# Performance work log

Hardware: AMD Instinct MI355X
Metric: run time of the kernel (lower is better)

The kernel has to match this reference:

```python
import jax, jax.numpy as jnp
import numpy as np

N, E, P, L, F, H, T = 6000, 72000, 2, 2, 64, 4, 64
NF_MLP = 256
DH = F // H
M = (L + 1) ** 2  # 9 spherical components for max_degree=2
DEG = np.array([l for l in range(L + 1) for _ in range(2 * l + 1)])  # degree of each m-component
EPS = 1e-6


def _deg_dense(x, W):
    # x: (n,P,M,Fin); W: (P,L+1,Fin,Fout). Separate feature mixing per (parity, degree),
    return jnp.einsum('npmf,pmfg->npmg', x, W[:, DEG])


def _eqv_layernorm(x):
    # Equivariant LayerNorm (no scale/bias): center the scalar (l=0) channel over features,
    # then divide each (parity, degree) block by the RMS (over features) of its per-degree norm.
    s = x[:, :, 0:1, :]
    x = x.at[:, :, 0:1, :].set(s - s.mean(axis=-1, keepdims=True))
    n2 = jnp.stack([(x[:, :, l * l:(l + 1) * (l + 1), :] ** 2).sum(axis=2) / (2 * l + 1)
                    for l in range(L + 1)], axis=2)  # (n,P,L+1,F)
    rms = jnp.sqrt(n2.mean(axis=-1, keepdims=True) + EPS)  # (n,P,L+1,1)
    return x / rms[:, :, DEG, :]


def _modulate(x, scale, shift):
    # modulate_E3adaLN: x * (1 + gamma) with gamma broadcast per degree; shift only on l=0 (scalar).
    y = x * (1.0 + scale[:, :, DEG, :])
    return y.at[:, :, 0:1, :].add(shift)


def _gate(factor, t):
    # broadcast_equivariant_multiplication: per-(parity,degree,feature) factor broadcast over m.
    return factor[:, :, DEG, :] * t


def _eqv_gelu(x):
    s = x[:, 0:1, 0:1, :]
    mask = jnp.abs(s) > 1e-4
    safe = jnp.where(mask, s, 1.0)
    g = jnp.where(mask, jax.nn.gelu(safe) / safe, 0.5)
    return x * g


def _forward(features_nodes, features_edges, features_time, cutoff_value,
             ln_t_scale, ln_t_bias, W_c, b_c, Wq, Wk, Wv, Wo, We_qk, We_v, W1, W2,
             src_idx, dst_idx):
    n = features_nodes.shape[0]
    # ---- AdaLN conditioning from time features ----
    mu = features_time.mean(-1, keepdims=True)
    var = ((features_time - mu) ** 2).mean(-1, keepdims=True)
    c = (features_time - mu) / jnp.sqrt(var + EPS) * ln_t_scale + ln_t_bias
    c = jax.nn.silu(c) @ W_c + b_c  # (n, 4*F*(L+1)*P + 2F)
    a = F * (L + 1) * P  # 384
    g1, b1, a1, g2, b2, a2 = jnp.split(c, [a, a + F, 2 * a + F, 3 * a + F, 3 * a + 2 * F], axis=-1)
    g1 = g1.reshape(n, P, L + 1, F); b1 = b1.reshape(n, 1, 1, F); a1 = a1.reshape(n, P, L + 1, F)
    g2 = g2.reshape(n, P, L + 1, F); b2 = b2.reshape(n, 1, 1, F); a2 = a2.reshape(n, P, L + 1, F)
    x_pre = _modulate(_eqv_layernorm(features_nodes), g1, b1)
    # ---- sparse graph equivariant self-attention ----
    q = _deg_dense(x_pre, Wq).reshape(n, P, M, H, DH)
    k = _deg_dense(x_pre, Wk).reshape(n, P, M, H, DH)
    v = _deg_dense(x_pre, Wv).reshape(n, P, M, H, DH)
    e_qk = jnp.einsum('eomf,fg->eomg', features_edges, We_qk).reshape(-1, 1, M, H, DH)
    e_v = jnp.einsum('eomf,fg->eomg', features_edges, We_v).reshape(-1, 1, M, H, DH)
    qe = q[dst_idx]
    ke = k[src_idx] * e_qk  # relative positional encoding on keys
    ve = v[src_idx] * e_v   # relative positional encoding on values
    logits = jnp.einsum('epmhd,epmhd->eh', qe, ke) / np.sqrt(P * M * DH)  # rotation-invariant
    lmax = jax.ops.segment_max(logits, dst_idx, num_segments=n)
    w = jnp.exp(logits - lmax[dst_idx]) * cutoff_value[:, None]  # cutoff-masked softmax weight
    denom = jax.ops.segment_sum(w, dst_idx, num_segments=n)
    attn = w / (denom[dst_idx] + 1e-9)  # (E,H)
    out = jax.ops.segment_sum(attn[:, None, None, :, None] * ve, dst_idx, num_segments=n)
    out = _deg_dense(out.reshape(n, P, M, F), Wo)
    # fallback to pre-attention features where segment_mean(cutoff) ~ 0 (isolated nodes)
    cnt = jax.ops.segment_sum(jnp.ones_like(cutoff_value), dst_idx, num_segments=n)
    mean_cut = jax.ops.segment_sum(cutoff_value, dst_idx, num_segments=n) / jnp.maximum(cnt, 1.0)
    post = jnp.where(mean_cut.reshape(-1, 1, 1, 1) < 1e-5, x_pre, out)
    x = features_nodes + _gate(a1, post)
    # ---- equivariant MLP ----
    x_pre2 = _modulate(_eqv_layernorm(x), g2, b2)
    h = _eqv_gelu(_deg_dense(x_pre2, W1))
    x = x + _gate(a2, _deg_dense(h, W2))
    return x  # node features; edge features pass through unchanged


def setup_inputs():
    key = jax.random.key(0)
    ks = jax.random.split(key, 16)
    CDIM = 4 * F * (L + 1) * P + 2 * F  # 1664
    return {
        'features_nodes': jax.random.normal(ks[0], (N, P, M, F), jnp.float32),
        'features_edges': jax.random.normal(ks[1], (E, 1, M, F), jnp.float32),
        'features_time': jax.random.normal(ks[2], (N, T), jnp.float32),
        'cutoff_value': jax.random.uniform(ks[3], (E,), jnp.float32),
        'ln_t_scale': jnp.ones((T,), jnp.float32),
        'ln_t_bias': jnp.zeros((T,), jnp.float32),
        'W_c': jax.random.normal(ks[4], (T, CDIM), jnp.float32) * 0.02,
        'b_c': jnp.zeros((CDIM,), jnp.float32),
        'Wq': jax.random.normal(ks[5], (P, L + 1, F, F), jnp.float32) / np.sqrt(F),
        'Wk': jax.random.normal(ks[6], (P, L + 1, F, F), jnp.float32) / np.sqrt(F),
        'Wv': jax.random.normal(ks[7], (P, L + 1, F, F), jnp.float32) / np.sqrt(F),
        'Wo': jax.random.normal(ks[8], (P, L + 1, F, F), jnp.float32) / np.sqrt(F),
        'We_qk': jax.random.normal(ks[9], (F, F), jnp.float32) / np.sqrt(F),
        'We_v': jax.random.normal(ks[10], (F, F), jnp.float32) / np.sqrt(F),
        'W1': jax.random.normal(ks[11], (P, L + 1, F, NF_MLP), jnp.float32) / np.sqrt(F),
        'W2': jax.random.normal(ks[12], (P, L + 1, NF_MLP, F), jnp.float32) / np.sqrt(NF_MLP),
        'src_idx': jax.random.randint(ks[13], (E,), 0, N),
        'dst_idx': jax.random.randint(ks[14], (E,), 0, N),
    }


def reference(features_nodes, features_edges, features_time, cutoff_value,
              ln_t_scale, ln_t_bias, W_c, b_c, Wq, Wk, Wv, Wo, We_qk, We_v, W1, W2,
              src_idx, dst_idx):
    return _forward(features_nodes, features_edges, features_time, cutoff_value,
                    ln_t_scale, ln_t_bias, W_c, b_c, Wq, Wk, Wv, Wo, We_qk, We_v, W1, W2,
                    src_idx, dst_idx)
```

## Files before the change

kernel.cpp:

```cpp
#include <hip/hip_runtime.h>
#include <hip/hip_fp16.h>
#include <math.h>


#define NN 6000
#define EE 72000

__device__ __forceinline__ float wsum(float v) {
#pragma unroll
  for (int o = 32; o >= 1; o >>= 1) v += __shfl_xor(v, o, 64);
  return v;
}
__device__ __forceinline__ int deg_of(int m) { return (m == 0) ? 0 : ((m < 4) ? 1 : 2); }
__device__ __forceinline__ unsigned fenc(float x) {
  unsigned u = __float_as_uint(x);
  return (u & 0x80000000u) ? ~u : (u | 0x80000000u);
}
__device__ __forceinline__ float fdec(unsigned k) {
  unsigned u = (k & 0x80000000u) ? (k & 0x7fffffffu) : ~k;
  return __uint_as_float(u);
}

__global__ __launch_bounds__(256) void k_ln_t(const float* __restrict__ ft,
                                              const float* __restrict__ lns,
                                              const float* __restrict__ lnb,
                                              float* __restrict__ sbuf) {
  int w = (blockIdx.x * 256 + threadIdx.x) >> 6;
  int lane = threadIdx.x & 63;
  float t = ft[(size_t)w * 64 + lane];
  float mu = wsum(t) * (1.f / 64.f);
  float d = t - mu;
  float var = wsum(d * d) * (1.f / 64.f);
  float cin = d * rsqrtf(var + 1e-6f) * lns[lane] + lnb[lane];
  sbuf[(size_t)w * 64 + lane] = cin / (1.f + expf(-cin));
}

__global__ __launch_bounds__(256) void k_cond_mm(const float* __restrict__ sbuf,
                                                 const float* __restrict__ Wc,
                                                 const float* __restrict__ bc,
                                                 float* __restrict__ c) {
  int n0 = blockIdx.x * 8;
  for (int jj = threadIdx.x; jj < 1664; jj += 256) {
    float acc[8] = {0, 0, 0, 0, 0, 0, 0, 0};
#pragma unroll 8
    for (int k2 = 0; k2 < 64; k2++) {
      float wv = Wc[(size_t)k2 * 1664 + jj];
#pragma unroll
      for (int nd = 0; nd < 8; nd++) acc[nd] += sbuf[(size_t)(n0 + nd) * 64 + k2] * wv;
    }
    float b = bc[jj];
#pragma unroll
    for (int nd = 0; nd < 8; nd++) c[(size_t)(n0 + nd) * 1664 + jj] = acc[nd] + b;
  }
}

__global__ __launch_bounds__(256) void k_lnmod(const float* __restrict__ xin,
                                               const float* __restrict__ c,
                                               float* __restrict__ xout,
                                               int goff, int boff) {
  int w = (blockIdx.x * 256 + threadIdx.x) >> 6;
  int lane = threadIdx.x & 63;
  int n = w >> 1, p = w & 1;
  const float* xb = xin + (size_t)w * 576 + lane;
  float x0 = xb[0], x1 = xb[64], x2 = xb[128], x3 = xb[192], x4 = xb[256];
  float x5 = xb[320], x6 = xb[384], x7 = xb[448], x8 = xb[512];
  float mu = wsum(x0) * (1.f / 64.f);
  x0 -= mu;
  float n20 = x0 * x0;
  float n21 = (x1 * x1 + x2 * x2 + x3 * x3) * (1.f / 3.f);
  float n22 = (x4 * x4 + x5 * x5 + x6 * x6 + x7 * x7 + x8 * x8) * (1.f / 5.f);
  n20 = wsum(n20) * (1.f / 64.f);
  n21 = wsum(n21) * (1.f / 64.f);
  n22 = wsum(n22) * (1.f / 64.f);
  float i0 = rsqrtf(n20 + 1e-6f), i1 = rsqrtf(n21 + 1e-6f), i2 = rsqrtf(n22 + 1e-6f);
  const float* cb = c + (size_t)n * 1664;
  float g0 = 1.f + cb[goff + p * 192 + lane];
  float g1 = 1.f + cb[goff + p * 192 + 64 + lane];
  float g2 = 1.f + cb[goff + p * 192 + 128 + lane];
  float bsh = cb[boff + lane];
  float* ob = xout + (size_t)w * 576 + lane;
  ob[0] = x0 * i0 * g0 + bsh;
  ob[64] = x1 * i1 * g1;
  ob[128] = x2 * i1 * g1;
  ob[192] = x3 * i1 * g1;
  ob[256] = x4 * i2 * g2;
  ob[320] = x5 * i2 * g2;
  ob[384] = x6 * i2 * g2;
  ob[448] = x7 * i2 * g2;
  ob[512] = x8 * i2 * g2;
}

__global__ __launch_bounds__(256) void k_count(const int* __restrict__ dst_idx,
                                               const float* __restrict__ cutoff,
                                               float* __restrict__ cnt,
                                               float* __restrict__ cutsum) {
  int e = blockIdx.x * 256 + threadIdx.x;
  if (e >= EE) return;
  int d = dst_idx[e];
  unsafeAtomicAdd(cnt + d, 1.f);
  unsafeAtomicAdd(cutsum + d, cutoff[e]);
}

__global__ __launch_bounds__(1024) void k_scan(const float* __restrict__ cnt,
                                               int* __restrict__ rowptr,
                                               int* __restrict__ fillc) {
  __shared__ int part[1024];
  int t = threadIdx.x;
  int base = t * 6;
  int lc[6];
  int s = 0;
#pragma unroll
  for (int i = 0; i < 6; i++) {
    int idx = base + i;
    int vv = (idx < NN) ? (int)(cnt[idx] + 0.5f) : 0;
    lc[i] = s;
    s += vv;
  }
  part[t] = s;
  __syncthreads();
  for (int o = 1; o < 1024; o <<= 1) {
    int vv = (t >= o) ? part[t - o] : 0;
    __syncthreads();
    part[t] += vv;
    __syncthreads();
  }
  int ex = (t == 0) ? 0 : part[t - 1];
#pragma unroll
  for (int i = 0; i < 6; i++) {
    int idx = base + i;
    if (idx < NN) {
      int p = ex + lc[i];
      rowptr[idx] = p;
      fillc[idx] = p;
    }
  }
  if (t == 1023) rowptr[NN] = part[1023];
}

__global__ __launch_bounds__(256) void k_fill(const int* __restrict__ dst_idx,
                                              const int* __restrict__ src_idx,
                                              const float* __restrict__ cutoff,
                                              int* __restrict__ fillc,
                                              int* __restrict__ eids,
                                              int* __restrict__ dsts,
                                              int* __restrict__ srcs,
                                              float* __restrict__ cuts) {
  int e = blockIdx.x * 256 + threadIdx.x;
  if (e >= EE) return;
  int d = dst_idx[e];
  int pos = atomicAdd(fillc + d, 1);
  eids[pos] = e;
  dsts[pos] = d;
  srcs[pos] = src_idx[e];
  cuts[pos] = cutoff[e];
}

__global__ __launch_bounds__(192) void k_qkv2(const float* __restrict__ xpre,
                                              const float* __restrict__ Wq,
                                              const float* __restrict__ Wk,
                                              const float* __restrict__ Wv,
                                              __half* __restrict__ qh,
                                              __half* __restrict__ kh,
                                              __half* __restrict__ vh) {
  __shared__ __align__(16) float xt[16 * 64];
  int pm = blockIdx.y;
  int p = pm / 9, dm = deg_of(pm % 9);
  int n0 = blockIdx.x * 16;
  int mat = threadIdx.x >> 6;
  int g = threadIdx.x & 63;
  for (int i = threadIdx.x; i < 1024; i += 192) {
    int r = i >> 6, f = i & 63;
    xt[i] = xpre[((size_t)(n0 + r) * 18 + pm) * 64 + f];
  }
  const float* Wsel = (mat == 0) ? Wq : ((mat == 1) ? Wk : Wv);
  const float* Wb = Wsel + (size_t)(p * 3 + dm) * 4096;
  __half* ob = (mat == 0) ? qh : ((mat == 1) ? kh : vh);
  float wreg[64];
#pragma unroll
  for (int f = 0; f < 64; f++) wreg[f] = Wb[f * 64 + g];
  __syncthreads();
  for (int r = 0; r < 16; r++) {
    float acc = 0.f;
#pragma unroll
    for (int f4 = 0; f4 < 16; f4++) {
      float4 a = *(const float4*)(xt + r * 64 + f4 * 4);
      acc += a.x * wreg[4 * f4] + a.y * wreg[4 * f4 + 1] + a.z * wreg[4 * f4 + 2] +
             a.w * wreg[4 * f4 + 3];
    }
    ob[((size_t)(n0 + r) * 18 + pm) * 64 + g] = __float2half(acc);
  }
}

__global__ __launch_bounds__(256) void k_edge(const float* __restrict__ fe,
                                              const float* __restrict__ Weqk,
                                              const float* __restrict__ Wev,
                                              const __half* __restrict__ qh,
                                              const __half* __restrict__ kh,
                                              const int* __restrict__ eids,
                                              const int* __restrict__ dsts,
                                              const int* __restrict__ srcs,
                                              __half* __restrict__ evh,
                                              float* __restrict__ logw,
                                              unsigned* __restrict__ lmax) {
  __shared__ __align__(16) float ft[16 * 576];
  int s0 = blockIdx.x * 16;
  int g = threadIdx.x & 63;
  int w = threadIdx.x >> 6;
  float wq[64], wv[64];
#pragma unroll
  for (int f = 0; f < 64; f++) {
    wq[f] = Weqk[f * 64 + g];
    wv[f] = Wev[f * 64 + g];
  }
  {
    int sl = threadIdx.x >> 4, j = threadIdx.x & 15;
    const float* sp = fe + (size_t)eids[s0 + sl] * 576;
#pragma unroll
    for (int i = 0; i < 9; i++) {
      *(float4*)(ft + sl * 576 + i * 64 + j * 4) = *(const float4*)(sp + i * 64 + j * 4);
    }
  }
  __syncthreads();
  for (int ss = 0; ss < 4; ss++) {
    int sl = w * 4 + ss;
    int s = s0 + sl;
    float eq[9];
#pragma unroll
    for (int m = 0; m < 9; m++) {
      float eqm = 0.f, evm = 0.f;
#pragma unroll
      for (int f4 = 0; f4 < 16; f4++) {
        float4 a = *(const float4*)(ft + sl * 576 + m * 64 + f4 * 4);
        eqm += a.x * wq[4 * f4] + a.y * wq[4 * f4 + 1] + a.z * wq[4 * f4 + 2] +
               a.w * wq[4 * f4 + 3];
        evm += a.x * wv[4 * f4] + a.y * wv[4 * f4 + 1] + a.z * wv[4 * f4 + 2] +
               a.w * wv[4 * f4 + 3];
      }
      eq[m] = eqm;
      evh[(size_t)s * 576 + m * 64 + g] = __float2half(evm);
    }
    int dst = __builtin_amdgcn_readfirstlane(dsts[s]);
    int src = __builtin_amdgcn_readfirstlane(srcs[s]);
    const __half* qb = qh + (size_t)dst * 1152 + g;
    const __half* kb = kh + (size_t)src * 1152 + g;
    float lacc = 0.f;
#pragma unroll
    for (int m = 0; m < 9; m++) {
      float qk = __half2float(qb[m * 64]) * __half2float(kb[m * 64]) +
                 __half2float(qb[m * 64 + 576]) * __half2float(kb[m * 64 + 576]);
      lacc += eq[m] * qk;
    }
    lacc *= 0.05892556509887896f;
    lacc += __shfl_xor(lacc, 8, 64);
    lacc += __shfl_xor(lacc, 4, 64);
    lacc += __shfl_xor(lacc, 2, 64);
    lacc += __shfl_xor(lacc, 1, 64);
    if ((g & 15) == 0) {
      int h = g >> 4;
      logw[(size_t)s * 4 + h] = lacc;
      atomicMax(lmax + (size_t)dst * 4 + h, fenc(lacc));
    }
  }
}

__global__ __launch_bounds__(256) void k_expw2(float* __restrict__ logw,
                                               const unsigned* __restrict__ lmax,
                                               const int* __restrict__ dsts,
                                               const float* __restrict__ cuts,
                                               float* __restrict__ denom) {
  int t = blockIdx.x * 256 + threadIdx.x;
  int s = t >> 2, h = t & 3;
  int dst = dsts[s];
  float wv = expf(logw[t] - fdec(lmax[(size_t)dst * 4 + h])) * cuts[s];
  logw[t] = wv;
  unsafeAtomicAdd(denom + (size_t)dst * 4 + h, wv);
}

__global__ __launch_bounds__(256) void k_fagg2(const __half* __restrict__ evh,
                                               const __half* __restrict__ vh,
                                               const int* __restrict__ srcs,
                                               const int* __restrict__ rowptr,
                                               const float* __restrict__ logw,
                                               const float* __restrict__ denom,
                                               float* __restrict__ attn_out) {
  int dst = (blockIdx.x * 256 + threadIdx.x) >> 6;
  int g = threadIdx.x & 63;
  int e0 = __builtin_amdgcn_readfirstlane(rowptr[dst]);
  int e1 = __builtin_amdgcn_readfirstlane(rowptr[dst + 1]);
  float invd = 1.f / (denom[(size_t)dst * 4 + (g >> 4)] + 1e-9f);
  float acc[18];
#pragma unroll
  for (int i = 0; i < 18; i++) acc[i] = 0.f;
  for (int s = e0; s < e1; s++) {
    float attn = logw[(size_t)s * 4 + (g >> 4)] * invd;
    int src = __builtin_amdgcn_readfirstlane(srcs[s]);
    const __half* eb = evh + (size_t)s * 576 + g;
    const __half* vb = vh + (size_t)src * 1152 + g;
#pragma unroll
    for (int m = 0; m < 9; m++) {
      float sc = attn * __half2float(eb[m * 64]);
      acc[m] += sc * __half2float(vb[m * 64]);
      acc[m + 9] += sc * __half2float(vb[m * 64 + 576]);
    }
  }
  float* ob = attn_out + (size_t)dst * 1152 + g;
#pragma unroll
  for (int m = 0; m < 9; m++) {
    ob[m * 64] = acc[m];
    ob[m * 64 + 576] = acc[m + 9];
  }
}

__global__ __launch_bounds__(256) void k_wo_post3(const float* __restrict__ attn_out,
                                                  const float* __restrict__ Wo,
                                                  const float* __restrict__ xpre,
                                                  const float* __restrict__ fnodes,
                                                  const float* __restrict__ c,
                                                  const float* __restrict__ cnt,
                                                  const float* __restrict__ cutsum,
                                                  float* __restrict__ out) {
  __shared__ __align__(16) float xt[16 * 64];
  int pm = blockIdx.y;
  int p = pm / 9, dm = deg_of(pm % 9);
  int n0 = blockIdx.x * 16;
  int g = threadIdx.x & 63, w = threadIdx.x >> 6;
  for (int i = threadIdx.x; i < 1024; i += 256) {
    int r = i >> 6, f = i & 63;
    xt[i] = attn_out[((size_t)(n0 + r) * 18 + pm) * 64 + f];
  }
  const float* Wb = Wo + (size_t)(p * 3 + dm) * 4096;
  float wreg[64];
#pragma unroll
  for (int f = 0; f < 64; f++) wreg[f] = Wb[f * 64 + g];
  __syncthreads();
  for (int i = 0; i < 4; i++) {
    int r = w * 4 + i;
    int n = n0 + r;
    float acc = 0.f;
#pragma unroll
    for (int f4 = 0; f4 < 16; f4++) {
      float4 a = *(const float4*)(xt + r * 64 + f4 * 4);
      acc += a.x * wreg[4 * f4] + a.y * wreg[4 * f4 + 1] + a.z * wreg[4 * f4 + 2] +
             a.w * wreg[4 * f4 + 3];
    }
    float mc = cutsum[n] / fmaxf(cnt[n], 1.f);
    size_t idx = ((size_t)n * 18 + pm) * 64 + g;
    float post = (mc < 1e-5f) ? xpre[idx] : acc;
    float a1v = c[(size_t)n * 1664 + 448 + (p * 3 + dm) * 64 + g];
    out[idx] = fnodes[idx] + a1v * post;
  }
}

__global__ __launch_bounds__(256) void k_mlp1(const float* __restrict__ xp2,
                                              const float* __restrict__ W1,
                                              float* __restrict__ h) {
  int n0 = blockIdx.x * 8;
  int j = threadIdx.x;
  float gate[8];
  {
    float acc[8] = {0, 0, 0, 0, 0, 0, 0, 0};
#pragma unroll 8
    for (int f = 0; f < 64; f++) {
      float wv = W1[(size_t)f * 256 + j];
#pragma unroll
      for (int nd = 0; nd < 8; nd++) acc[nd] += xp2[(size_t)(n0 + nd) * 1152 + f] * wv;
    }
#pragma unroll
    for (int nd = 0; nd < 8; nd++) {
      float s = acc[nd];
      float g = (fabsf(s) > 1e-4f)
                    ? 0.5f * (1.f + tanhf(0.7978845608028654f * (s + 0.044715f * s * s * s)))
                    : 0.5f;
      gate[nd] = g;
      h[(size_t)(n0 + nd) * 4608 + j] = s * g;
    }
  }
  for (int pm = 1; pm < 18; pm++) {
    int p = pm / 9, mm = pm % 9, dm = deg_of(mm);
    const float* wb = W1 + (size_t)(p * 3 + dm) * 16384;
    float acc[8] = {0, 0, 0, 0, 0, 0, 0, 0};
#pragma unroll 8
    for (int f = 0; f < 64; f++) {
      float wv = wb[(size_t)f * 256 + j];
#pragma unroll
      for (int nd = 0; nd < 8; nd++)
        acc[nd] += xp2[(size_t)(n0 + nd) * 1152 + pm * 64 + f] * wv;
    }
#pragma unroll
    for (int nd = 0; nd < 8; nd++)
      h[(size_t)(n0 + nd) * 4608 + pm * 256 + j] = acc[nd] * gate[nd];
  }
}

__global__ __launch_bounds__(256) void k_mlp2(const float* __restrict__ h,
                                              const float* __restrict__ W2,
                                              const float* __restrict__ c,
                                              float* __restrict__ out) {
  int n0 = blockIdx.x * 8;
  int g = threadIdx.x & 63;
  int pr = threadIdx.x >> 6;
  for (int pm = pr; pm < 18; pm += 4) {
    int p = pm / 9, mm = pm % 9, dm = deg_of(mm);
    const float* wb = W2 + (size_t)(p * 3 + dm) * 16384;
    float acc[8] = {0, 0, 0, 0, 0, 0, 0, 0};
#pragma unroll 8
    for (int k = 0; k < 256; k++) {
      float wv = wb[(size_t)k * 64 + g];
#pragma unroll
      for (int nd = 0; nd < 8; nd++)
        acc[nd] += h[(size_t)(n0 + nd) * 4608 + pm * 256 + k] * wv;
    }
#pragma unroll
    for (int nd = 0; nd < 8; nd++) {
      int n = n0 + nd;
      size_t idx = ((size_t)n * 18 + pm) * 64 + g;
      out[idx] += c[(size_t)n * 1664 + 1280 + (p * 3 + dm) * 64 + g] * acc[nd];
    }
  }
}

#define OFF_C 0UL
#define OFF_XPRE 39936000UL
#define OFF_QH 67584000UL
#define OFF_KH 81408000UL
#define OFF_VH 95232000UL
#define OFF_EVH 109056000UL
#define OFF_ATTN 67584000UL
#define OFF_H 67584000UL
#define OFF_SBUF 192000000UL
#define OFF_LOGW 193536000UL
#define OFF_LMAX 194688000UL
#define OFF_DENOM 194784000UL
#define OFF_CNT 194880000UL
#define OFF_CUTSUM 194904000UL
#define OFF_ROWPTR 194928000UL
#define OFF_FILLC 194952064UL
#define OFF_EIDS 194976064UL
#define OFF_DSTS 195264064UL
#define OFF_SRCS 195552064UL
#define OFF_CUTS 195840064UL
#define WS_NEEDED 196128064UL

extern "C" void kernel_launch(void* const* d_in, const int* in_sizes, int n_in,
                              void* d_out, int out_size, void* d_ws, size_t ws_size,
                              hipStream_t stream) {
  const float* f_nodes = (const float*)d_in[0];
  const float* f_edges = (const float*)d_in[1];
  const float* f_time = (const float*)d_in[2];
  const float* cutoff = (const float*)d_in[3];
  const float* ln_s = (const float*)d_in[4];
  const float* ln_b = (const float*)d_in[5];
  const float* W_c = (const float*)d_in[6];
  const float* b_c = (const float*)d_in[7];
  const float* Wq = (const float*)d_in[8];
  const float* Wk = (const float*)d_in[9];
  const float* Wv = (const float*)d_in[10];
  const float* Wo = (const float*)d_in[11];
  const float* We_qk = (const float*)d_in[12];
  const float* We_v = (const float*)d_in[13];
  const float* W1 = (const float*)d_in[14];
  const float* W2 = (const float*)d_in[15];
  const int* src_idx = (const int*)d_in[16];
  const int* dst_idx = (const int*)d_in[17];
  float* out = (float*)d_out;
  char* ws = (char*)d_ws;
  if (ws_size < WS_NEEDED) return;

  float* c = (float*)(ws + OFF_C);
  float* xpre = (float*)(ws + OFF_XPRE);
  __half* qh = (__half*)(ws + OFF_QH);
  __half* kh = (__half*)(ws + OFF_KH);
  __half* vh = (__half*)(ws + OFF_VH);
  __half* evh = (__half*)(ws + OFF_EVH);
  float* attn_out = (float*)(ws + OFF_ATTN);
  float* hbuf = (float*)(ws + OFF_H);
  float* sbuf = (float*)(ws + OFF_SBUF);
  float* logw = (float*)(ws + OFF_LOGW);
  unsigned* lmax = (unsigned*)(ws + OFF_LMAX);
  float* denom = (float*)(ws + OFF_DENOM);
  float* cnt = (float*)(ws + OFF_CNT);
  float* cutsum = (float*)(ws + OFF_CUTSUM);
  int* rowptr = (int*)(ws + OFF_ROWPTR);
  int* fillc = (int*)(ws + OFF_FILLC);
  int* eids = (int*)(ws + OFF_EIDS);
  int* dsts = (int*)(ws + OFF_DSTS);
  int* srcs = (int*)(ws + OFF_SRCS);
  float* cuts = (float*)(ws + OFF_CUTS);

  hipMemsetAsync(ws + OFF_LMAX, 0, 240000, stream);

  k_ln_t<<<1500, 256, 0, stream>>>(f_time, ln_s, ln_b, sbuf);
  k_count<<<282, 256, 0, stream>>>(dst_idx, cutoff, cnt, cutsum);
  k_cond_mm<<<750, 256, 0, stream>>>(sbuf, W_c, b_c, c);
  k_scan<<<1, 1024, 0, stream>>>(cnt, rowptr, fillc);
  k_fill<<<282, 256, 0, stream>>>(dst_idx, src_idx, cutoff, fillc, eids, dsts, srcs,
                                  cuts);
  k_lnmod<<<3000, 256, 0, stream>>>(f_nodes, c, xpre, 0, 384);

  k_qkv2<<<dim3(375, 18), 192, 0, stream>>>(xpre, Wq, Wk, Wv, qh, kh, vh);

  k_edge<<<4500, 256, 0, stream>>>(f_edges, We_qk, We_v, qh, kh, eids, dsts, srcs, evh,
                                   logw, lmax);
  k_expw2<<<1125, 256, 0, stream>>>(logw, lmax, dsts, cuts, denom);
  k_fagg2<<<1500, 256, 0, stream>>>(evh, vh, srcs, rowptr, logw, denom, attn_out);
  k_wo_post3<<<dim3(375, 18), 256, 0, stream>>>(attn_out, Wo, xpre, f_nodes, c, cnt,
                                                cutsum, out);

  k_lnmod<<<3000, 256, 0, stream>>>(out, c, xpre, 832, 1216);
  k_mlp1<<<750, 256, 0, stream>>>(xpre, W1, hbuf);
  k_mlp2<<<750, 256, 0, stream>>>(hbuf, W2, c, out);
}
```

Measured before the change: 1.080 ms.

## Fuse MLP up/down projections into one kernel keeping hidden in LDS

Merges the two MLP kernels into one. Each block handles 16 nodes, keeps W1/W2 slices in registers per (parity, degree), computes the hidden activations into shared memory, and reduces the second projection across waves. This removes the 4608-wide global hidden buffer write and read. It also stages the conditioning input in shared memory for the cond matmul. The costs are 128 weight registers per thread, fewer blocks (375), and many barriers per m-component.

Result: slower. 1.269 ms (+17.5%).

```diff
diff --git a/kernel.cpp b/kernel.cpp
--- a/kernel.cpp
+++ b/kernel.cpp
@@ -39,14 +39,17 @@
                                                  const float* __restrict__ Wc,
                                                  const float* __restrict__ bc,
                                                  float* __restrict__ c) {
+  __shared__ __align__(16) float st[8 * 64];
   int n0 = blockIdx.x * 8;
+  for (int i = threadIdx.x; i < 512; i += 256) st[i] = sbuf[(size_t)n0 * 64 + i];
+  __syncthreads();
   for (int jj = threadIdx.x; jj < 1664; jj += 256) {
     float acc[8] = {0, 0, 0, 0, 0, 0, 0, 0};
 #pragma unroll 8
     for (int k2 = 0; k2 < 64; k2++) {
       float wv = Wc[(size_t)k2 * 1664 + jj];
 #pragma unroll
-      for (int nd = 0; nd < 8; nd++) acc[nd] += sbuf[(size_t)(n0 + nd) * 64 + k2] * wv;
+      for (int nd = 0; nd < 8; nd++) acc[nd] += st[nd * 64 + k2] * wv;
     }
     float b = bc[jj];
 #pragma unroll
@@ -351,70 +354,76 @@
   }
 }
 
-__global__ __launch_bounds__(256) void k_mlp1(const float* __restrict__ xp2,
-                                              const float* __restrict__ W1,
-                                              float* __restrict__ h) {
-  int n0 = blockIdx.x * 8;
-  int j = threadIdx.x;
-  float gate[8];
-  {
-    float acc[8] = {0, 0, 0, 0, 0, 0, 0, 0};
-#pragma unroll 8
-    for (int f = 0; f < 64; f++) {
-      float wv = W1[(size_t)f * 256 + j];
-#pragma unroll
-      for (int nd = 0; nd < 8; nd++) acc[nd] += xp2[(size_t)(n0 + nd) * 1152 + f] * wv;
-    }
-#pragma unroll
-    for (int nd = 0; nd < 8; nd++) {
-      float s = acc[nd];
-      float g = (fabsf(s) > 1e-4f)
-                    ? 0.5f * (1.f + tanhf(0.7978845608028654f * (s + 0.044715f * s * s * s)))
-                    : 0.5f;
-      gate[nd] = g;
-      h[(size_t)(n0 + nd) * 4608 + j] = s * g;
-    }
-  }
-  for (int pm = 1; pm < 18; pm++) {
-    int p = pm / 9, mm = pm % 9, dm = deg_of(mm);
-    const float* wb = W1 + (size_t)(p * 3 + dm) * 16384;
-    float acc[8] = {0, 0, 0, 0, 0, 0, 0, 0};
-#pragma unroll 8
-    for (int f = 0; f < 64; f++) {
-      float wv = wb[(size_t)f * 256 + j];
-#pragma unroll
-      for (int nd = 0; nd < 8; nd++)
-        acc[nd] += xp2[(size_t)(n0 + nd) * 1152 + pm * 64 + f] * wv;
-    }
-#pragma unroll
-    for (int nd = 0; nd < 8; nd++)
-      h[(size_t)(n0 + nd) * 4608 + pm * 256 + j] = acc[nd] * gate[nd];
-  }
-}
-
-__global__ __launch_bounds__(256) void k_mlp2(const float* __restrict__ h,
-                                              const float* __restrict__ W2,
-                                              const float* __restrict__ c,
-                                              float* __restrict__ out) {
-  int n0 = blockIdx.x * 8;
-  int g = threadIdx.x & 63;
-  int pr = threadIdx.x >> 6;
-  for (int pm = pr; pm < 18; pm += 4) {
-    int p = pm / 9, mm = pm % 9, dm = deg_of(mm);
-    const float* wb = W2 + (size_t)(p * 3 + dm) * 16384;
-    float acc[8] = {0, 0, 0, 0, 0, 0, 0, 0};
-#pragma unroll 8
-    for (int k = 0; k < 256; k++) {
-      float wv = wb[(size_t)k * 64 + g];
-#pragma unroll
-      for (int nd = 0; nd < 8; nd++)
-        acc[nd] += h[(size_t)(n0 + nd) * 4608 + pm * 256 + k] * wv;
-    }
-#pragma unroll
-    for (int nd = 0; nd < 8; nd++) {
-      int n = n0 + nd;
-      size_t idx = ((size_t)n * 18 + pm) * 64 + g;
-      out[idx] += c[(size_t)n * 1664 + 1280 + (p * 3 + dm) * 64 + g] * acc[nd];
+__global__ __launch_bounds__(256) void k_mlp(const float* __restrict__ xp2,
+                                             const float* __restrict__ W1,
+                                             const float* __restrict__ W2,
+                                             const float* __restrict__ c,
+                                             float* __restrict__ out) {
+  __shared__ __align__(16) float xt[16 * 64];
+  __shared__ float gate[16 * 256];
+  __shared__ __align__(16) float ht[16 * 256];
+  __shared__ float po[4][16 * 64];
+  int n0 = blockIdx.x * 16;
+  int w = threadIdx.x >> 6, g = threadIdx.x & 63;
+  for (int p = 0; p < 2; p++) {
+    for (int dm = 0; dm < 3; dm++) {
+      const float* w1b = W1 + (size_t)(p * 3 + dm) * 16384;
+      const float* w2b = W2 + (size_t)(p * 3 + dm) * 16384;
+      float w1reg[64], w2reg[64];
+#pragma unroll
+      for (int f = 0; f < 64; f++) w1reg[f] = w1b[(size_t)f * 256 + w * 64 + g];
+#pragma unroll
+      for (int k = 0; k < 64; k++) w2reg[k] = w2b[(size_t)(w * 64 + k) * 64 + g];
+      int mlo = (dm == 0) ? 0 : ((dm == 1) ? 1 : 4);
+      int mhi = (dm == 0) ? 1 : ((dm == 1) ? 4 : 9);
+      for (int mm = mlo; mm < mhi; mm++) {
+        int pm = p * 9 + mm;
+        __syncthreads();
+        for (int i = threadIdx.x; i < 1024; i += 256) {
+          int r = i >> 6, f = i & 63;
+          xt[i] = xp2[((size_t)(n0 + r) * 18 + pm) * 64 + f];
+        }
+        __syncthreads();
+        for (int r = 0; r < 16; r++) {
+          float acc = 0.f;
+#pragma unroll
+          for (int f4 = 0; f4 < 16; f4++) {
+            float4 a = *(const float4*)(xt + r * 64 + f4 * 4);
+            acc += a.x * w1reg[4 * f4] + a.y * w1reg[4 * f4 + 1] +
+                   a.z * w1reg[4 * f4 + 2] + a.w * w1reg[4 * f4 + 3];
+          }
+          int j = r * 256 + w * 64 + g;
+          if (pm == 0) {
+            float gt = (fabsf(acc) > 1e-4f)
+                           ? 0.5f * (1.f + tanhf(0.7978845608028654f *
+                                                 (acc + 0.044715f * acc * acc * acc)))
+                           : 0.5f;
+            gate[j] = gt;
+            ht[j] = acc * gt;
+          } else {
+            ht[j] = acc * gate[j];
+          }
+        }
+        __syncthreads();
+        for (int r = 0; r < 16; r++) {
+          float acc = 0.f;
+#pragma unroll
+          for (int k4 = 0; k4 < 16; k4++) {
+            float4 a = *(const float4*)(ht + r * 256 + w * 64 + k4 * 4);
+            acc += a.x * w2reg[4 * k4] + a.y * w2reg[4 * k4 + 1] +
+                   a.z * w2reg[4 * k4 + 2] + a.w * w2reg[4 * k4 + 3];
+          }
+          po[w][r * 64 + g] = acc;
+        }
+        __syncthreads();
+        for (int i = threadIdx.x; i < 1024; i += 256) {
+          int r = i >> 6, gg = i & 63;
+          float s2 = po[0][i] + po[1][i] + po[2][i] + po[3][i];
+          int n = n0 + r;
+          size_t idx = ((size_t)n * 18 + pm) * 64 + gg;
+          out[idx] += c[(size_t)n * 1664 + 1280 + (p * 3 + dm) * 64 + gg] * s2;
+        }
+      }
     }
   }
 }
@@ -426,7 +435,6 @@
 #define OFF_VH 95232000UL
 #define OFF_EVH 109056000UL
 #define OFF_ATTN 67584000UL
-#define OFF_H 67584000UL
 #define OFF_SBUF 192000000UL
 #define OFF_LOGW 193536000UL
 #define OFF_LMAX 194688000UL
@@ -473,7 +481,6 @@
   __half* vh = (__half*)(ws + OFF_VH);
   __half* evh = (__half*)(ws + OFF_EVH);
   float* attn_out = (float*)(ws + OFF_ATTN);
-  float* hbuf = (float*)(ws + OFF_H);
   float* sbuf = (float*)(ws + OFF_SBUF);
   float* logw = (float*)(ws + OFF_LOGW);
   unsigned* lmax = (unsigned*)(ws + OFF_LMAX);
@@ -507,6 +514,5 @@
                                                 cutsum, out);
 
   k_lnmod<<<3000, 256, 0, stream>>>(out, c, xpre, 832, 1216);
-  k_mlp1<<<750, 256, 0, stream>>>(xpre, W1, hbuf);
-  k_mlp2<<<750, 256, 0, stream>>>(hbuf, W2, c, out);
-}
+  k_mlp<<<375, 256, 0, stream>>>(xpre, W1, W2, c, out);
+}
```
